# Kernel tuning notes

Measured on AMD Instinct MI355X. Metric: run time of the kernel, lower is better.

## Reference

```python
import jax, jax.numpy as jnp
import numpy as np

C = 512          # in_channels
N1 = 8192        # level-1 nodes
N2 = 131072      # level-2 nodes
N = 1 + N1 + N2  # total nodes (node 0 = root)
E = 1_000_000    # edges
STEP = 10        # ceil(1/ratio), ratio=0.1
K1 = (N1 + STEP - 1) // STEP   # 820 level-1 clusters
K2 = 4 * K1                    # max level-2 clusters (4 centers per parent)
M = 1 + K1 + K2                # coarse node count


def setup_inputs() -> dict:
    key = jax.random.key(0)
    ks = jax.random.split(key, 6)
    x = jax.random.normal(ks[0], (N, C), dtype=jnp.float32)
    edge_index = jax.random.randint(ks[1], (2, E), 0, N, dtype=jnp.int32)
    # fixed hierarchy layout: node 0 root, nodes 1..N1 level-1, rest level-2
    node_type = jnp.concatenate([jnp.zeros(1, jnp.int32),
                                 jnp.ones(N1, jnp.int32),
                                 jnp.full((N2,), 2, jnp.int32)])
    # tree: level-2 nodes point to a level-1 parent (global idx in [1, N1])
    tree = jax.random.randint(ks[2], (N,), 1, N1 + 1, dtype=jnp.int32)
    x_y_index = jax.random.uniform(ks[3], (N, 2), dtype=jnp.float32) * 100.0
    weight_1 = jax.random.normal(ks[4], (1, C), dtype=jnp.float32) * 0.04
    weight_2 = jax.random.normal(ks[5], (1, C), dtype=jnp.float32) * 0.04
    return {"x": x, "edge_index": edge_index, "node_type": node_type,
            "tree": tree, "x_y_index": x_y_index,
            "weight_1": weight_1, "weight_2": weight_2}


def _pair_dist(a, b):
    # a:[m,3], b:[n,3]; xy euclidean distance + |fitness diff| (euclidean_dist)
    dxy = jnp.sqrt(jnp.sum((a[:, None, :2] - b[None, :, :2]) ** 2, axis=-1))
    df = jnp.abs(a[:, None, 2] - b[None, :, 2])
    return dxy + df


def reference(x, edge_index, node_type, tree, x_y_index, weight_1, weight_2):
    x1, x2 = x[1:1 + N1], x[1 + N1:]
    xy1, xy2 = x_y_index[1:1 + N1], x_y_index[1 + N1:]

    # ---- level-1: fitness, threshold selection, cluster by nearest center ----
    f1 = jnp.tanh(jnp.sum(x1 * weight_1, axis=-1) / jnp.linalg.norm(weight_1))
    xyf1 = jnp.concatenate([xy1, f1[:, None]], axis=-1)          # [N1,3]
    order1 = jnp.argsort(f1)
    thr1 = order1[::STEP]                                        # [K1]
    d1 = _pair_dist(xyf1[thr1], xyf1)                            # [K1,N1]
    cluster_1 = jnp.argmin(d1, axis=0).astype(jnp.int32)         # [N1]

    # ---- level-2: fitness, 4 centers per parent cluster, nearest-center ----
    f2 = jnp.tanh(jnp.sum(x2 * weight_2, axis=-1) / jnp.linalg.norm(weight_2))
    xyf2 = jnp.concatenate([xy2, f2[:, None]], axis=-1)          # [N2,3]
    tree2 = tree[1 + N1:]
    parents = cluster_1[tree2 - jnp.min(tree2)]                  # [N2] in [0,K1)
    # pick 4 lowest-fitness members of each parent cluster as centers
    # (static-shape deterministic variant of random.sample over sorted fitness)
    comp_key = parents.astype(jnp.float32) * 4.0 + f2            # fitness in (-1,1)
    order2 = jnp.argsort(comp_key)
    p_sorted = parents[order2]
    counts = jax.ops.segment_sum(jnp.ones((N2,), jnp.int32), parents, K1)
    starts = jnp.concatenate([jnp.zeros(1, jnp.int32), jnp.cumsum(counts)[:-1]])
    rank = jnp.arange(N2, dtype=jnp.int32) - starts[p_sorted]
    row = jnp.where(rank < 4, p_sorted, K1)                      # overflow -> dummy row
    cand = jnp.full((K1 + 1, 4), -1, jnp.int32)
    cand = cand.at[row, jnp.clip(rank, 0, 3)].set(order2.astype(jnp.int32))[:K1]
    valid = cand >= 0                                            # [K1,4]
    cand_xyf = xyf2[jnp.where(valid, cand, 0)]                   # [K1,4,3]
    a = cand_xyf[parents]                                        # [N2,4,3]
    d2 = (jnp.sqrt(jnp.sum((a[..., :2] - xy2[:, None, :]) ** 2, axis=-1))
          + jnp.abs(a[..., 2] - f2[:, None]))
    d2 = jnp.where(valid[parents], d2, jnp.inf)
    local = jnp.argmin(d2, axis=1).astype(jnp.int32)             # [N2] in [0,4)
    cluster_2 = parents * 4 + local                              # [N2]

    # ---- merge cluster ids: [root | level-1 clusters | level-2 clusters] ----
    cluster = jnp.concatenate([jnp.zeros(1, jnp.int32),
                               cluster_1 + 1,
                               cluster_2 + 1 + K1])              # [N] in [0,M)

    # ---- scatter-mean pooling of features and coordinates ----
    cnt = jnp.maximum(jax.ops.segment_sum(jnp.ones((N, 1), x.dtype), cluster, M), 1.0)
    x_pool = jax.ops.segment_sum(x, cluster, M) / cnt            # [M,C]
    new_xy = jax.ops.segment_sum(x_y_index, cluster, M) / cnt    # [M,2]

    # ---- coarsen adjacency (self loops added on fine graph first) ----
    rows = jnp.concatenate([edge_index[0], jnp.arange(N, dtype=jnp.int32)])
    cols = jnp.concatenate([edge_index[1], jnp.arange(N, dtype=jnp.int32)])
    A = jnp.zeros((M, M), x.dtype).at[cluster[rows], cluster[cols]].add(1.0)

    new_node_type = jnp.concatenate([jnp.zeros(1, jnp.int32),
                                     jnp.ones(K1, jnp.int32),
                                     jnp.full((K2,), 2, jnp.int32)])
    new_tree = jnp.concatenate([jnp.full((1,), -1, jnp.int32),
                                jnp.zeros(K1, jnp.int32),
                                jnp.repeat(jnp.arange(1, K1 + 1, dtype=jnp.int32), 4)])
    fitness = jnp.concatenate([jnp.zeros(1, x.dtype), f1, f2])
    batch = jnp.zeros((M,), jnp.int32)
    return x_pool, A, batch, cluster, new_node_type, new_tree, fitness, new_xy
```

## Files before the change

kernel.cpp:

```cpp
#include <hip/hip_runtime.h>
#include <cstdint>
#include <cstddef>
#include <math.h>

#define C_     512
#define N1_    8192
#define N2_    131072
#define NTOT   139265
#define E_     1000000
#define K1_    820
#define K2_    3280
#define M_     4101
#define NB2    256
#define NBM    273

#define OFF_XPOOL   0ull
#define OFF_A       2099712ull
#define OFF_BATCH   18917913ull
#define OFF_CLUSTER 18922014ull
#define OFF_NNT     19061279ull
#define OFF_NTREE   19065380ull
#define OFF_FIT     19069481ull
#define OFF_NXY     19208746ull
#define OUT_TOTAL   19216948ull


__global__ void k_zero4(float4* __restrict__ p, long n4, float* __restrict__ tail, int ntail,
                        float* __restrict__ out) {
    long i = (long)blockIdx.x * blockDim.x + threadIdx.x;
    long stride = (long)gridDim.x * blockDim.x;
    float4 z = make_float4(0.f, 0.f, 0.f, 0.f);
    for (long k = i; k < n4; k += stride) p[k] = z;
    if (blockIdx.x == 0 && threadIdx.x < ntail) tail[threadIdx.x] = 0.f;
    if (i < M_) {
        out[OFF_NNT + i] = (i == 0) ? 0.0f : (i <= K1_ ? 1.0f : 2.0f);
        out[OFF_NTREE + i] = (i == 0) ? -1.0f : (i <= K1_ ? 0.0f : (float)(1 + (i - 1 - K1_) / 4));
        out[OFF_BATCH + i] = 0.0f;
        if (i == 0) out[OFF_FIT] = 0.0f;
    }
}

__device__ __forceinline__ float pairwise_combine(float r) {
    float o;
    o = __shfl_xor(r, 1, 64);  r = __fadd_rn(r, o);
    o = __shfl_xor(r, 2, 64);  r = __fadd_rn(r, o);
    o = __shfl_xor(r, 4, 64);  r = __fadd_rn(r, o);
    o = __shfl_xor(r, 8, 64);  r = __fadd_rn(r, o);
    o = __shfl_xor(r, 16, 64); r = __fadd_rn(r, o);
    return r;
}

__global__ void k_fit(const float* __restrict__ x, const float* __restrict__ w,
                      int rowOff, float* __restrict__ fs, float* __restrict__ fitOut) {
    __shared__ float wbuf[C_];
    __shared__ float xbuf[8][C_];
    for (int j = threadIdx.x; j < C_; j += 256) wbuf[j] = w[j];
    int wv = threadIdx.x >> 6, lane = threadIdx.x & 63;
    int rowA = blockIdx.x * 8 + wv * 2;
    const float4* rA = (const float4*)(x + (size_t)(rowOff + rowA) * C_);
    const float4* rB = (const float4*)(x + (size_t)(rowOff + rowA + 1) * C_);
    float4* xa = (float4*)xbuf[wv * 2];
    float4* xb = (float4*)xbuf[wv * 2 + 1];
    xa[lane] = rA[lane];
    xa[lane + 64] = rA[lane + 64];
    xb[lane] = rB[lane];
    xb[lane + 64] = rB[lane + 64];
    __syncthreads();
    int hl = lane & 31;
    int base = (hl >> 3) * 128 + (hl & 7);
    const float* xr = xbuf[wv * 2 + (lane >> 5)];
    float nv = wbuf[base];
    float nr = __fmul_rn(nv, nv);
    float r = __fmul_rn(xr[base], wbuf[base]);
    #pragma unroll
    for (int i = 1; i < 16; ++i) {
        int c = base + 8 * i;
        float u = wbuf[c];
        nr = __fadd_rn(nr, __fmul_rn(u, u));
        r = __fadd_rn(r, __fmul_rn(xr[c], u));
    }
    nr = pairwise_combine(nr);
    r = pairwise_combine(r);
    if (hl == 0) {
        float nrm = __fsqrt_rn(nr);
        float q = __fdiv_rn(r, nrm);
        float f = (float)tanh((double)q);
        int gw = rowA + (lane >> 5);
        fs[gw] = f;
        fitOut[gw] = f;
    }
}

#define RJ 512
__global__ void k_rank_partial(const float* __restrict__ f1s, int* __restrict__ rank) {
    __shared__ float buf[RJ];
    int i = blockIdx.x * 256 + threadIdx.x;
    int jbase = blockIdx.y * RJ;
    for (int j = threadIdx.x; j < RJ; j += 256) buf[j] = f1s[jbase + j];
    float fi = f1s[i];
    __syncthreads();
    int r = 0;
    #pragma unroll 8
    for (int j = 0; j < RJ; ++j) {
        float fj = buf[j];
        int jj = jbase + j;
        r += (int)((fj < fi) || (fj == fi && jj < i));
    }
    atomicAdd(&rank[i], r);
}

__global__ void k_thr(const int* __restrict__ rank, const float* __restrict__ xy,
                      const float* __restrict__ f1s, float* __restrict__ thrXYF) {
    int i = blockIdx.x * blockDim.x + threadIdx.x;
    if (i >= N1_) return;
    int r = rank[i];
    if (r % 10 == 0) {
        int k = r / 10;
        thrXYF[3 * k + 0] = xy[(size_t)(1 + i) * 2 + 0];
        thrXYF[3 * k + 1] = xy[(size_t)(1 + i) * 2 + 1];
        thrXYF[3 * k + 2] = f1s[i];
    }
}

__device__ __forceinline__ float pair_dist_f32(float ax, float ay, float af,
                                               float bx, float by, float bf) {
    float dx = __fsub_rn(ax, bx);
    float dy = __fsub_rn(ay, by);
    float dx2 = __fmul_rn(dx, dx);
    float dy2 = __fmul_rn(dy, dy);
    float ss = __fadd_rn(dx2, dy2);
    float dxy = __fsqrt_rn(ss);
    float df = fabsf(__fsub_rn(af, bf));
    return __fadd_rn(dxy, df);
}

__global__ void k_cluster1(const float* __restrict__ xy, const float* __restrict__ f1s,
                           const float* __restrict__ thrXYF,
                           int* __restrict__ cluster1, int* __restrict__ clusterAll,
                           float* __restrict__ outCluster, int* __restrict__ cntM) {
    __shared__ float t[K1_ * 3];
    for (int j = threadIdx.x; j < K1_ * 3; j += blockDim.x) t[j] = thrXYF[j];
    __syncthreads();
    if (blockIdx.x == 0 && threadIdx.x == 0) {
        clusterAll[0] = 0; outCluster[0] = 0.0f;
        atomicAdd(&cntM[0], 1);
    }
    int gw = blockIdx.x * (blockDim.x >> 6) + (threadIdx.x >> 6);
    int lane = threadIdx.x & 63;
    if (gw >= N1_) return;
    float xi = xy[(size_t)(1 + gw) * 2 + 0];
    float yi = xy[(size_t)(1 + gw) * 2 + 1];
    float fi = f1s[gw];
    float best = INFINITY; int bk = 0x7fffffff;
    for (int k = lane; k < K1_; k += 64) {
        float d = pair_dist_f32(t[3 * k + 0], t[3 * k + 1], t[3 * k + 2], xi, yi, fi);
        if (d < best || (d == best && k < bk)) { best = d; bk = k; }
    }
    for (int off = 32; off > 0; off >>= 1) {
        float ob = __shfl_down(best, off, 64);
        int ok = __shfl_down(bk, off, 64);
        if (ob < best || (ob == best && ok < bk)) { best = ob; bk = ok; }
    }
    if (lane == 0) {
        cluster1[gw] = bk;
        clusterAll[1 + gw] = bk + 1;
        outCluster[1 + gw] = (float)(bk + 1);
        atomicAdd(&cntM[bk + 1], 1);
    }
}

__global__ void k_mintree(const int* __restrict__ tree, int* __restrict__ minTree) {
    int i = blockIdx.x * blockDim.x + threadIdx.x;
    if (i >= N2_) return;
    int v = tree[1 + N1_ + i];
    for (int off = 32; off > 0; off >>= 1) v = min(v, __shfl_down(v, off, 64));
    if ((threadIdx.x & 63) == 0) atomicMin(minTree, v);
}

__global__ void k_parents(const int* __restrict__ tree, const int* __restrict__ cluster1,
                          const int* __restrict__ minTree,
                          int* __restrict__ parents, int* __restrict__ countP) {
    int i = blockIdx.x * blockDim.x + threadIdx.x;
    if (i >= N2_) return;
    int p = cluster1[tree[1 + N1_ + i] - minTree[0]];
    parents[i] = p;
    atomicAdd(&countP[p], 1);
}

__global__ void k_scan(const int* __restrict__ cnt, int* __restrict__ start, int n) {
    __shared__ int partial[1024];
    int t = threadIdx.x;
    int per = (n + 1023) / 1024;
    int lo = t * per;
    int hi = lo + per; if (hi > n) hi = n;
    int s = 0;
    if (lo < n) for (int i = lo; i < hi; ++i) s += cnt[i];
    partial[t] = s;
    __syncthreads();
    for (int off = 1; off < 1024; off <<= 1) {
        int v = (t >= off) ? partial[t - off] : 0;
        __syncthreads();
        partial[t] += v;
        __syncthreads();
    }
    int base = (t > 0) ? partial[t - 1] : 0;
    if (lo < n) for (int i = lo; i < hi; ++i) { start[i] = base; base += cnt[i]; }
    if (t == 1023) start[n] = partial[1023];
}

__global__ void kA_count(const int* __restrict__ parents, int* __restrict__ bc) {
    __shared__ int hist[K1_];
    for (int j = threadIdx.x; j < K1_; j += 512) hist[j] = 0;
    __syncthreads();
    int i = blockIdx.x * 512 + threadIdx.x;
    atomicAdd(&hist[parents[i]], 1);
    __syncthreads();
    for (int j = threadIdx.x; j < K1_; j += 512) bc[(size_t)j * NB2 + blockIdx.x] = hist[j];
}

__global__ void kA_scan(const int* __restrict__ startP, int* __restrict__ bc) {
    int p = blockIdx.x * 256 + threadIdx.x;
    if (p >= K1_) return;
    int run = startP[p];
    int* row = bc + (size_t)p * NB2;
    for (int b = 0; b < NB2; ++b) { int t = row[b]; row[b] = run; run += t; }
}

__global__ void kA_place(const int* __restrict__ parents, const int* __restrict__ bc,
                         int* __restrict__ plist) {
    __shared__ int par[512];
    int i = blockIdx.x * 512 + threadIdx.x;
    int p = parents[i];
    par[threadIdx.x] = p;
    __syncthreads();
    int rank = 0;
    for (int j = 0; j < (int)threadIdx.x; ++j) rank += (par[j] == p);
    plist[bc[(size_t)p * NB2 + blockIdx.x] + rank] = i;
}

__global__ void kM_count(const int* __restrict__ clusterAll, int* __restrict__ bc) {
    __shared__ int hist[M_];
    for (int j = threadIdx.x; j < M_; j += 512) hist[j] = 0;
    __syncthreads();
    int i = blockIdx.x * 512 + threadIdx.x;
    if (i < NTOT) atomicAdd(&hist[clusterAll[i]], 1);
    __syncthreads();
    for (int j = threadIdx.x; j < M_; j += 512) bc[(size_t)j * NBM + blockIdx.x] = hist[j];
}

__global__ void kM_scan(const int* __restrict__ startM, int* __restrict__ bc) {
    int c = blockIdx.x * 256 + threadIdx.x;
    if (c >= M_) return;
    int run = startM[c];
    int* row = bc + (size_t)c * NBM;
    for (int b = 0; b < NBM; ++b) { int t = row[b]; row[b] = run; run += t; }
}

__global__ void kM_place(const int* __restrict__ clusterAll, const int* __restrict__ bc,
                         int* __restrict__ lst) {
    __shared__ int par[512];
    int i = blockIdx.x * 512 + threadIdx.x;
    int c = (i < NTOT) ? clusterAll[i] : -1;
    par[threadIdx.x] = c;
    __syncthreads();
    if (i >= NTOT) return;
    int rank = 0;
    for (int j = 0; j < (int)threadIdx.x; ++j) rank += (par[j] == c);
    lst[bc[(size_t)c * NBM + blockIdx.x] + rank] = i;
}

__global__ void k_top4(const int* __restrict__ startP, const int* __restrict__ plist,
                       const float* __restrict__ f2s, int* __restrict__ cand) {
    int p = blockIdx.x * (blockDim.x >> 6) + (threadIdx.x >> 6);
    int lane = threadIdx.x & 63;
    if (p >= K1_) return;
    int lo = startP[p], hi = startP[p + 1];
    float base = (float)(4 * p);
    float bk[4] = {INFINITY, INFINITY, INFINITY, INFINITY};
    int bi[4] = {-1, -1, -1, -1};
    for (int q = lo + lane; q < hi; q += 64) {
        int idx = plist[q];
        float key = __fadd_rn(base, f2s[idx]);
        for (int j = 0; j < 4; ++j) {
            bool less = (key < bk[j]) || (key == bk[j] && (unsigned)idx < (unsigned)bi[j]);
            if (less) {
                for (int r = 3; r > j; --r) { bk[r] = bk[r - 1]; bi[r] = bi[r - 1]; }
                bk[j] = key; bi[j] = idx;
                break;
            }
        }
    }
    for (int off = 1; off < 64; off <<= 1) {
        float ok_[4]; int oi[4];
        for (int j = 0; j < 4; ++j) {
            ok_[j] = __shfl_xor(bk[j], off, 64);
            oi[j]  = __shfl_xor(bi[j], off, 64);
        }
        float nk[4]; int ni[4];
        int ia = 0, ib = 0;
        for (int j = 0; j < 4; ++j) {
            bool takeA = (bk[ia] < ok_[ib]) ||
                         (bk[ia] == ok_[ib] && (unsigned)bi[ia] <= (unsigned)oi[ib]);
            if (takeA) { nk[j] = bk[ia]; ni[j] = bi[ia]; ++ia; }
            else       { nk[j] = ok_[ib]; ni[j] = oi[ib]; ++ib; }
        }
        for (int j = 0; j < 4; ++j) { bk[j] = nk[j]; bi[j] = ni[j]; }
    }
    if (lane == 0) {
        for (int j = 0; j < 4; ++j) cand[4 * p + j] = bi[j];
    }
}

__global__ void k_cluster2(const float* __restrict__ xy, const float* __restrict__ f2s,
                           const int* __restrict__ parents, const int* __restrict__ cand,
                           int* __restrict__ clusterAll, float* __restrict__ outCluster,
                           int* __restrict__ cntM) {
    int i = blockIdx.x * blockDim.x + threadIdx.x;
    if (i >= N2_) return;
    int p = parents[i];
    float xi = xy[(size_t)(1 + N1_ + i) * 2 + 0];
    float yi = xy[(size_t)(1 + N1_ + i) * 2 + 1];
    float fi = f2s[i];
    float best = INFINITY; int bj = 0;
    for (int j = 0; j < 4; ++j) {
        int cidx = cand[4 * p + j];
        float d;
        if (cidx < 0) {
            d = INFINITY;
        } else {
            float ax = xy[(size_t)(1 + N1_ + cidx) * 2 + 0];
            float ay = xy[(size_t)(1 + N1_ + cidx) * 2 + 1];
            float af = f2s[cidx];
            d = pair_dist_f32(ax, ay, af, xi, yi, fi);
        }
        if (d < best) { best = d; bj = j; }
    }
    int c2 = p * 4 + bj;
    int c = c2 + 1 + K1_;
    clusterAll[1 + N1_ + i] = c;
    outCluster[1 + N1_ + i] = (float)c;
    atomicAdd(&cntM[c], 1);
}

__global__ void k_pool(const float* __restrict__ x, const float* __restrict__ xy,
                       const int* __restrict__ startM, const int* __restrict__ clusterList,
                       float* __restrict__ out) {
    int m = blockIdx.x;
    int lo = startM[m], hi = startM[m + 1];
    int t = threadIdx.x;
    double s0 = 0.0, s1 = 0.0, s2 = 0.0, s3 = 0.0, sx = 0.0, sy = 0.0;
    int q = lo;
    for (; q + 1 < hi; q += 2) {
        int n0 = clusterList[q];
        int n1 = clusterList[q + 1];
        float4 a = ((const float4*)(x + (size_t)n0 * C_))[t];
        float4 b = ((const float4*)(x + (size_t)n1 * C_))[t];
        s0 += (double)a.x; s1 += (double)a.y; s2 += (double)a.z; s3 += (double)a.w;
        s0 += (double)b.x; s1 += (double)b.y; s2 += (double)b.z; s3 += (double)b.w;
        if (t == 0) sx += (double)xy[(size_t)n0 * 2 + 0] + (double)xy[(size_t)n1 * 2 + 0];
        if (t == 1) sy += (double)xy[(size_t)n0 * 2 + 1] + (double)xy[(size_t)n1 * 2 + 1];
    }
    if (q < hi) {
        int n0 = clusterList[q];
        float4 a = ((const float4*)(x + (size_t)n0 * C_))[t];
        s0 += (double)a.x; s1 += (double)a.y; s2 += (double)a.z; s3 += (double)a.w;
        if (t == 0) sx += (double)xy[(size_t)n0 * 2 + 0];
        if (t == 1) sy += (double)xy[(size_t)n0 * 2 + 1];
    }
    double cnt = (double)((hi - lo) > 0 ? (hi - lo) : 1);
    float4* xp = (float4*)(out + OFF_XPOOL + (size_t)m * C_);
    xp[t] = make_float4((float)(s0 / cnt), (float)(s1 / cnt),
                        (float)(s2 / cnt), (float)(s3 / cnt));
    if (t == 0) out[OFF_NXY + 2 * (size_t)m + 0] = (float)(sx / cnt);
    if (t == 1) out[OFF_NXY + 2 * (size_t)m + 1] = (float)(sy / cnt);
}

__global__ void k_edges(const int* __restrict__ ei, const int* __restrict__ clusterAll,
                        float* __restrict__ A) {
    int i = blockIdx.x * blockDim.x + threadIdx.x;
    if (i < E_) {
        int r = clusterAll[ei[i]];
        int c = clusterAll[ei[E_ + i]];
        atomicAdd(&A[(size_t)r * M_ + c], 1.0f);
    } else {
        int n = i - E_;
        if (n < NTOT) {
            int c = clusterAll[n];
            atomicAdd(&A[(size_t)c * M_ + c], 1.0f);
        }
    }
}

extern "C" void kernel_launch(void* const* d_in, const int* in_sizes, int n_in,
                              void* d_out, int out_size, void* d_ws, size_t ws_size,
                              hipStream_t stream) {
    const float* x    = (const float*)d_in[0];
    const int*   ei   = (const int*)d_in[1];
    const int*   tree = (const int*)d_in[3];
    const float* xy   = (const float*)d_in[4];
    const float* w1   = (const float*)d_in[5];
    const float* w2   = (const float*)d_in[6];
    float* out = (float*)d_out;

    char* p = (char*)d_ws;
    auto alloc = [&](size_t nbytes) -> char* {
        char* r = p;
        p += (nbytes + 255) & ~(size_t)255;
        return r;
    };
    float*  f1s        = (float*)alloc((size_t)N1_ * 4);
    float*  f2s        = (float*)alloc((size_t)N2_ * 4);
    float*  thrXYF     = (float*)alloc((size_t)K1_ * 3 * 4);
    int*    cluster1   = (int*)alloc((size_t)N1_ * 4);
    int*    clusterAll = (int*)alloc((size_t)NTOT * 4);
    int*    parentsA   = (int*)alloc((size_t)N2_ * 4);
    int*    plist      = (int*)alloc((size_t)N2_ * 4);
    int*    clusterLst = (int*)alloc((size_t)NTOT * 4);
    int*    startP     = (int*)alloc((size_t)(K1_ + 1) * 4);
    int*    startM     = (int*)alloc((size_t)(M_ + 1) * 4);
    int*    bcP        = (int*)alloc((size_t)K1_ * NB2 * 4);
    int*    bcM        = (int*)alloc((size_t)M_ * NBM * 4);
    size_t zeroInts = (size_t)(K1_ + M_ + N1_);
    char*   zeroBlk    = alloc(zeroInts * 4);
    int*    countP     = (int*)zeroBlk;
    int*    cntM       = countP + K1_;
    int*    rankArr    = cntM + M_;
    int*    cand       = (int*)alloc((size_t)K1_ * 4 * 4);
    int*    minTree    = (int*)alloc(4);

    hipMemsetAsync(zeroBlk, 0, zeroInts * 4, stream);
    hipMemsetAsync(minTree, 0x7F, 4, stream);

    {
        long nA = (long)M_ * M_;
        long n4 = nA / 4;
        int ntail = (int)(nA - n4 * 4);
        float* A = out + OFF_A;
        k_zero4<<<4096, 256, 0, stream>>>((float4*)A, n4, A + n4 * 4, ntail, out);
    }

    k_fit<<<N1_ / 8, 256, 0, stream>>>(x, w1, 1, f1s, out + OFF_FIT + 1);
    k_fit<<<N2_ / 8, 256, 0, stream>>>(x, w2, 1 + N1_, f2s, out + OFF_FIT + 1 + N1_);
    {
        dim3 g(N1_ / 256, N1_ / RJ);
        k_rank_partial<<<g, 256, 0, stream>>>(f1s, rankArr);
    }
    k_thr<<<N1_ / 256, 256, 0, stream>>>(rankArr, xy, f1s, thrXYF);
    k_cluster1<<<N1_ / 4, 256, 0, stream>>>(xy, f1s, thrXYF, cluster1, clusterAll,
                                            out + OFF_CLUSTER, cntM);
    k_mintree<<<N2_ / 256, 256, 0, stream>>>(tree, minTree);
    k_parents<<<N2_ / 256, 256, 0, stream>>>(tree, cluster1, minTree, parentsA, countP);
    k_scan<<<1, 1024, 0, stream>>>(countP, startP, K1_);
    kA_count<<<NB2, 512, 0, stream>>>(parentsA, bcP);
    kA_scan<<<(K1_ + 255) / 256, 256, 0, stream>>>(startP, bcP);
    kA_place<<<NB2, 512, 0, stream>>>(parentsA, bcP, plist);
    k_top4<<<(K1_ + 3) / 4, 256, 0, stream>>>(startP, plist, f2s, cand);
    k_cluster2<<<N2_ / 256, 256, 0, stream>>>(xy, f2s, parentsA, cand, clusterAll,
                                              out + OFF_CLUSTER, cntM);
    k_scan<<<1, 1024, 0, stream>>>(cntM, startM, M_);
    kM_count<<<NBM, 512, 0, stream>>>(clusterAll, bcM);
    kM_scan<<<(M_ + 255) / 256, 256, 0, stream>>>(startM, bcM);
    kM_place<<<NBM, 512, 0, stream>>>(clusterAll, bcM, clusterLst);
    k_pool<<<M_, 128, 0, stream>>>(x, xy, startM, clusterLst, out);
    k_edges<<<(E_ + NTOT + 255) / 256, 256, 0, stream>>>(ei, clusterAll, out + OFF_A);
}
```

Measured before the change: 798.3 us.

## Fuse whole pipeline into one persistent kernel with software grid barriers

Replaces roughly twenty separate kernel launches with one persistent kernel of 240 blocks. Stages are separated by atomic-counter grid barriers. Along the way it overlaps A-matrix zeroing and the min-tree reduction with the fitness pass, replaces the count-then-scan steps with flattened chunked scans, and runs edge scatter and pooling back to back. This removes launch gaps and tail effects. The cost is reduced parallelism in some stages (240 blocks), barrier spin overhead, and deadlock if not all blocks are co-resident.

```diff
diff --git a/kernel.cpp b/kernel.cpp
--- a/kernel.cpp
+++ b/kernel.cpp
@@ -13,6 +13,19 @@
 #define M_     4101
 #define NB2    256
 #define NBM    273
+#define FLATP  209920
+#define CHP    820
+#define FLATM  1119573
+#define CHM    4374
+#define NCHS   256
+
+#define G_     240
+#define BLK_   512
+#define FITB   210
+#define ZB     30
+#define ZTOT   15360
+#define NG16   8704
+#define PADC   544
 
 #define OFF_XPOOL   0ull
 #define OFF_A       2099712ull
@@ -25,19 +38,36 @@
 #define OUT_TOTAL   19216948ull
 
 
-__global__ void k_zero4(float4* __restrict__ p, long n4, float* __restrict__ tail, int ntail,
-                        float* __restrict__ out) {
-    long i = (long)blockIdx.x * blockDim.x + threadIdx.x;
-    long stride = (long)gridDim.x * blockDim.x;
-    float4 z = make_float4(0.f, 0.f, 0.f, 0.f);
-    for (long k = i; k < n4; k += stride) p[k] = z;
-    if (blockIdx.x == 0 && threadIdx.x < ntail) tail[threadIdx.x] = 0.f;
-    if (i < M_) {
-        out[OFF_NNT + i] = (i == 0) ? 0.0f : (i <= K1_ ? 1.0f : 2.0f);
-        out[OFF_NTREE + i] = (i == 0) ? -1.0f : (i <= K1_ ? 0.0f : (float)(1 + (i - 1 - K1_) / 4));
-        out[OFF_BATCH + i] = 0.0f;
-        if (i == 0) out[OFF_FIT] = 0.0f;
-    }
+struct MegaArgs {
+    const float* x; const int* ei; const int* tree; const float* xy;
+    const float* w1; const float* w2;
+    float* out;
+    float* f1s; float* f2s; float* thrXYF;
+    int* cluster1; int* clusterAll; int* parentsA; int* plist; int* clusterLst;
+    int* bcP; int* bcM;
+    int* totP; int* coffP; int* totM; int* coffM;
+    int* rankArr; int* minTreeNeg;
+    int* cand;
+    int* barCnt; int* barGen;
+};
+
+__device__ __forceinline__ void gbar(int* cnt, int* gen) {
+    __syncthreads();
+    if (threadIdx.x == 0) {
+        __threadfence();
+        int g = __hip_atomic_load(gen, __ATOMIC_RELAXED, __HIP_MEMORY_SCOPE_AGENT);
+        int old = __hip_atomic_fetch_add(cnt, 1, __ATOMIC_ACQ_REL, __HIP_MEMORY_SCOPE_AGENT);
+        if (old == (int)gridDim.x - 1) {
+            __hip_atomic_store(cnt, 0, __ATOMIC_RELAXED, __HIP_MEMORY_SCOPE_AGENT);
+            __hip_atomic_fetch_add(gen, 1, __ATOMIC_RELEASE, __HIP_MEMORY_SCOPE_AGENT);
+        } else {
+            while (__hip_atomic_load(gen, __ATOMIC_RELAXED, __HIP_MEMORY_SCOPE_AGENT) == g) {
+                __builtin_amdgcn_s_sleep(1);
+            }
+        }
+        __threadfence();
+    }
+    __syncthreads();
 }
 
 __device__ __forceinline__ float pairwise_combine(float r) {
@@ -48,78 +78,6 @@
     o = __shfl_xor(r, 8, 64);  r = __fadd_rn(r, o);
     o = __shfl_xor(r, 16, 64); r = __fadd_rn(r, o);
     return r;
-}
-
-__global__ void k_fit(const float* __restrict__ x, const float* __restrict__ w,
-                      int rowOff, float* __restrict__ fs, float* __restrict__ fitOut) {
-    __shared__ float wbuf[C_];
-    __shared__ float xbuf[8][C_];
-    for (int j = threadIdx.x; j < C_; j += 256) wbuf[j] = w[j];
-    int wv = threadIdx.x >> 6, lane = threadIdx.x & 63;
-    int rowA = blockIdx.x * 8 + wv * 2;
-    const float4* rA = (const float4*)(x + (size_t)(rowOff + rowA) * C_);
-    const float4* rB = (const float4*)(x + (size_t)(rowOff + rowA + 1) * C_);
-    float4* xa = (float4*)xbuf[wv * 2];
-    float4* xb = (float4*)xbuf[wv * 2 + 1];
-    xa[lane] = rA[lane];
-    xa[lane + 64] = rA[lane + 64];
-    xb[lane] = rB[lane];
-    xb[lane + 64] = rB[lane + 64];
-    __syncthreads();
-    int hl = lane & 31;
-    int base = (hl >> 3) * 128 + (hl & 7);
-    const float* xr = xbuf[wv * 2 + (lane >> 5)];
-    float nv = wbuf[base];
-    float nr = __fmul_rn(nv, nv);
-    float r = __fmul_rn(xr[base], wbuf[base]);
-    #pragma unroll
-    for (int i = 1; i < 16; ++i) {
-        int c = base + 8 * i;
-        float u = wbuf[c];
-        nr = __fadd_rn(nr, __fmul_rn(u, u));
-        r = __fadd_rn(r, __fmul_rn(xr[c], u));
-    }
-    nr = pairwise_combine(nr);
-    r = pairwise_combine(r);
-    if (hl == 0) {
-        float nrm = __fsqrt_rn(nr);
-        float q = __fdiv_rn(r, nrm);
-        float f = (float)tanh((double)q);
-        int gw = rowA + (lane >> 5);
-        fs[gw] = f;
-        fitOut[gw] = f;
-    }
-}
-
-#define RJ 512
-__global__ void k_rank_partial(const float* __restrict__ f1s, int* __restrict__ rank) {
-    __shared__ float buf[RJ];
-    int i = blockIdx.x * 256 + threadIdx.x;
-    int jbase = blockIdx.y * RJ;
-    for (int j = threadIdx.x; j < RJ; j += 256) buf[j] = f1s[jbase + j];
-    float fi = f1s[i];
-    __syncthreads();
-    int r = 0;
-    #pragma unroll 8
-    for (int j = 0; j < RJ; ++j) {
-        float fj = buf[j];
-        int jj = jbase + j;
-        r += (int)((fj < fi) || (fj == fi && jj < i));
-    }
-    atomicAdd(&rank[i], r);
-}
-
-__global__ void k_thr(const int* __restrict__ rank, const float* __restrict__ xy,
-                      const float* __restrict__ f1s, float* __restrict__ thrXYF) {
-    int i = blockIdx.x * blockDim.x + threadIdx.x;
-    if (i >= N1_) return;
-    int r = rank[i];
-    if (r % 10 == 0) {
-        int k = r / 10;
-        thrXYF[3 * k + 0] = xy[(size_t)(1 + i) * 2 + 0];
-        thrXYF[3 * k + 1] = xy[(size_t)(1 + i) * 2 + 1];
-        thrXYF[3 * k + 2] = f1s[i];
-    }
 }
 
 __device__ __forceinline__ float pair_dist_f32(float ax, float ay, float af,
@@ -134,259 +92,416 @@
     return __fadd_rn(dxy, df);
 }
 
-__global__ void k_cluster1(const float* __restrict__ xy, const float* __restrict__ f1s,
-                           const float* __restrict__ thrXYF,
-                           int* __restrict__ cluster1, int* __restrict__ clusterAll,
-                           float* __restrict__ outCluster, int* __restrict__ cntM) {
-    __shared__ float t[K1_ * 3];
-    for (int j = threadIdx.x; j < K1_ * 3; j += blockDim.x) t[j] = thrXYF[j];
+__device__ __forceinline__ int block_incl_scan512(int v, int* sm) {
+    sm[threadIdx.x] = v;
     __syncthreads();
-    if (blockIdx.x == 0 && threadIdx.x == 0) {
-        clusterAll[0] = 0; outCluster[0] = 0.0f;
-        atomicAdd(&cntM[0], 1);
-    }
-    int gw = blockIdx.x * (blockDim.x >> 6) + (threadIdx.x >> 6);
-    int lane = threadIdx.x & 63;
-    if (gw >= N1_) return;
-    float xi = xy[(size_t)(1 + gw) * 2 + 0];
-    float yi = xy[(size_t)(1 + gw) * 2 + 1];
-    float fi = f1s[gw];
-    float best = INFINITY; int bk = 0x7fffffff;
-    for (int k = lane; k < K1_; k += 64) {
-        float d = pair_dist_f32(t[3 * k + 0], t[3 * k + 1], t[3 * k + 2], xi, yi, fi);
-        if (d < best || (d == best && k < bk)) { best = d; bk = k; }
-    }
-    for (int off = 32; off > 0; off >>= 1) {
-        float ob = __shfl_down(best, off, 64);
-        int ok = __shfl_down(bk, off, 64);
-        if (ob < best || (ob == best && ok < bk)) { best = ob; bk = ok; }
-    }
-    if (lane == 0) {
-        cluster1[gw] = bk;
-        clusterAll[1 + gw] = bk + 1;
-        outCluster[1 + gw] = (float)(bk + 1);
-        atomicAdd(&cntM[bk + 1], 1);
-    }
+    for (int off = 1; off < 512; off <<= 1) {
+        int y = ((int)threadIdx.x >= off) ? sm[threadIdx.x - off] : 0;
+        __syncthreads();
+        sm[threadIdx.x] += y;
+        __syncthreads();
+    }
+    return sm[threadIdx.x];
 }
 
-__global__ void k_mintree(const int* __restrict__ tree, int* __restrict__ minTree) {
-    int i = blockIdx.x * blockDim.x + threadIdx.x;
-    if (i >= N2_) return;
-    int v = tree[1 + N1_ + i];
-    for (int off = 32; off > 0; off >>= 1) v = min(v, __shfl_down(v, off, 64));
-    if ((threadIdx.x & 63) == 0) atomicMin(minTree, v);
-}
-
-__global__ void k_parents(const int* __restrict__ tree, const int* __restrict__ cluster1,
-                          const int* __restrict__ minTree,
-                          int* __restrict__ parents, int* __restrict__ countP) {
-    int i = blockIdx.x * blockDim.x + threadIdx.x;
-    if (i >= N2_) return;
-    int p = cluster1[tree[1 + N1_ + i] - minTree[0]];
-    parents[i] = p;
-    atomicAdd(&countP[p], 1);
-}
-
-__global__ void k_scan(const int* __restrict__ cnt, int* __restrict__ start, int n) {
-    __shared__ int partial[1024];
-    int t = threadIdx.x;
-    int per = (n + 1023) / 1024;
-    int lo = t * per;
-    int hi = lo + per; if (hi > n) hi = n;
-    int s = 0;
-    if (lo < n) for (int i = lo; i < hi; ++i) s += cnt[i];
-    partial[t] = s;
-    __syncthreads();
-    for (int off = 1; off < 1024; off <<= 1) {
-        int v = (t >= off) ? partial[t - off] : 0;
-        __syncthreads();
-        partial[t] += v;
-        __syncthreads();
-    }
-    int base = (t > 0) ? partial[t - 1] : 0;
-    if (lo < n) for (int i = lo; i < hi; ++i) { start[i] = base; base += cnt[i]; }
-    if (t == 1023) start[n] = partial[1023];
-}
-
-__global__ void kA_count(const int* __restrict__ parents, int* __restrict__ bc) {
-    __shared__ int hist[K1_];
-    for (int j = threadIdx.x; j < K1_; j += 512) hist[j] = 0;
-    __syncthreads();
-    int i = blockIdx.x * 512 + threadIdx.x;
-    atomicAdd(&hist[parents[i]], 1);
-    __syncthreads();
-    for (int j = threadIdx.x; j < K1_; j += 512) bc[(size_t)j * NB2 + blockIdx.x] = hist[j];
-}
-
-__global__ void kA_scan(const int* __restrict__ startP, int* __restrict__ bc) {
-    int p = blockIdx.x * 256 + threadIdx.x;
-    if (p >= K1_) return;
-    int run = startP[p];
-    int* row = bc + (size_t)p * NB2;
-    for (int b = 0; b < NB2; ++b) { int t = row[b]; row[b] = run; run += t; }
-}
-
-__global__ void kA_place(const int* __restrict__ parents, const int* __restrict__ bc,
-                         int* __restrict__ plist) {
-    __shared__ int par[512];
-    int i = blockIdx.x * 512 + threadIdx.x;
-    int p = parents[i];
-    par[threadIdx.x] = p;
-    __syncthreads();
-    int rank = 0;
-    for (int j = 0; j < (int)threadIdx.x; ++j) rank += (par[j] == p);
-    plist[bc[(size_t)p * NB2 + blockIdx.x] + rank] = i;
-}
-
-__global__ void kM_count(const int* __restrict__ clusterAll, int* __restrict__ bc) {
-    __shared__ int hist[M_];
-    for (int j = threadIdx.x; j < M_; j += 512) hist[j] = 0;
-    __syncthreads();
-    int i = blockIdx.x * 512 + threadIdx.x;
-    if (i < NTOT) atomicAdd(&hist[clusterAll[i]], 1);
-    __syncthreads();
-    for (int j = threadIdx.x; j < M_; j += 512) bc[(size_t)j * NBM + blockIdx.x] = hist[j];
-}
-
-__global__ void kM_scan(const int* __restrict__ startM, int* __restrict__ bc) {
-    int c = blockIdx.x * 256 + threadIdx.x;
-    if (c >= M_) return;
-    int run = startM[c];
-    int* row = bc + (size_t)c * NBM;
-    for (int b = 0; b < NBM; ++b) { int t = row[b]; row[b] = run; run += t; }
-}
-
-__global__ void kM_place(const int* __restrict__ clusterAll, const int* __restrict__ bc,
-                         int* __restrict__ lst) {
-    __shared__ int par[512];
-    int i = blockIdx.x * 512 + threadIdx.x;
-    int c = (i < NTOT) ? clusterAll[i] : -1;
-    par[threadIdx.x] = c;
-    __syncthreads();
-    if (i >= NTOT) return;
-    int rank = 0;
-    for (int j = 0; j < (int)threadIdx.x; ++j) rank += (par[j] == c);
-    lst[bc[(size_t)c * NBM + blockIdx.x] + rank] = i;
-}
-
-__global__ void k_top4(const int* __restrict__ startP, const int* __restrict__ plist,
-                       const float* __restrict__ f2s, int* __restrict__ cand) {
-    int p = blockIdx.x * (blockDim.x >> 6) + (threadIdx.x >> 6);
-    int lane = threadIdx.x & 63;
-    if (p >= K1_) return;
-    int lo = startP[p], hi = startP[p + 1];
-    float base = (float)(4 * p);
-    float bk[4] = {INFINITY, INFINITY, INFINITY, INFINITY};
-    int bi[4] = {-1, -1, -1, -1};
-    for (int q = lo + lane; q < hi; q += 64) {
-        int idx = plist[q];
-        float key = __fadd_rn(base, f2s[idx]);
+__global__ void __launch_bounds__(BLK_, 2) k_mega(MegaArgs a) {
+    __shared__ float smem_f[PADC * 17];
+    int* smem_i = (int*)smem_f;
+    const int tid = threadIdx.x;
+    const int bid = blockIdx.x;
+    const int wv = tid >> 6, lane = tid & 63;
+
+    if ((bid & 7) != 3) {
+        int fidx = bid - (bid >> 3) - (((bid & 7) > 3) ? 1 : 0);
+        float* wbuf = smem_f;
+        float* xbuf = smem_f + PADC;
+        for (int g = fidx; g < NG16; g += FITB) {
+            const float* w = (g < 512) ? a.w1 : a.w2;
+            if (tid < 128) {
+                float4 v = ((const float4*)w)[tid];
+                ((float4*)wbuf)[((tid >> 5) * 34) + (tid & 31)] = v;
+            }
+            {
+                int r0 = 2 * wv, r1 = r0 + 1;
+                const float4* rA = (const float4*)(a.x + (size_t)(1 + 16 * g + r0) * C_);
+                const float4* rB = (const float4*)(a.x + (size_t)(1 + 16 * g + r1) * C_);
+                float4* xa = (float4*)(xbuf + (size_t)r0 * PADC);
+                float4* xb = (float4*)(xbuf + (size_t)r1 * PADC);
+                int j0 = lane, j1 = lane + 64;
+                int d0 = ((j0 >> 5) * 34) + (j0 & 31);
+                int d1 = ((j1 >> 5) * 34) + (j1 & 31);
+                xa[d0] = rA[j0]; xa[d1] = rA[j1];
+                xb[d0] = rB[j0]; xb[d1] = rB[j1];
+            }
+            __syncthreads();
+            {
+                int hl = lane & 31;
+                int basep = ((hl >> 3) * 136) + (hl & 7);
+                const float* xr = xbuf + (size_t)(2 * wv + (lane >> 5)) * PADC;
+                float nv = wbuf[basep];
+                float nr = __fmul_rn(nv, nv);
+                float r = __fmul_rn(xr[basep], wbuf[basep]);
+                #pragma unroll
+                for (int i = 1; i < 16; ++i) {
+                    int c = basep + 8 * i;
+                    float u = wbuf[c];
+                    nr = __fadd_rn(nr, __fmul_rn(u, u));
+                    r = __fadd_rn(r, __fmul_rn(xr[c], u));
+                }
+                nr = pairwise_combine(nr);
+                r = pairwise_combine(r);
+                if (hl == 0) {
+                    float nrm = __fsqrt_rn(nr);
+                    float q = __fdiv_rn(r, nrm);
+                    float f = (float)tanh((double)q);
+                    int row16 = 16 * g + 2 * wv + (lane >> 5);
+                    if (row16 < N1_) a.f1s[row16] = f;
+                    else             a.f2s[row16 - N1_] = f;
+                    a.out[OFF_FIT + 1 + row16] = f;
+                }
+            }
+            __syncthreads();
+        }
+    } else {
+        int ztid = (bid >> 3) * BLK_ + tid;
+        float* A = a.out + OFF_A;
+        const long n4 = ((long)M_ * M_) >> 2;
+        float4 z = make_float4(0.f, 0.f, 0.f, 0.f);
+        for (long k4 = ztid; k4 < n4; k4 += ZTOT) ((float4*)A)[k4] = z;
+        if (ztid == 0) {
+            A[(size_t)n4 * 4] = 0.f;
+            a.clusterAll[0] = 0;
+            a.out[OFF_CLUSTER] = 0.0f;
+            a.out[OFF_FIT] = 0.0f;
+        }
+        if (ztid < M_) {
+            a.out[OFF_NNT + ztid] = (ztid == 0) ? 0.0f : (ztid <= K1_ ? 1.0f : 2.0f);
+            a.out[OFF_NTREE + ztid] = (ztid == 0) ? -1.0f
+                                    : (ztid <= K1_ ? 0.0f : (float)(1 + (ztid - 1 - K1_) / 4));
+            a.out[OFF_BATCH + ztid] = 0.0f;
+        }
+        int u = 0;
+        for (int i = ztid; i < N2_; i += ZTOT) {
+            int v = a.tree[1 + N1_ + i];
+            u = max(u, 0x7FFFFFFF - v);
+        }
+        for (int off = 32; off > 0; off >>= 1) u = max(u, __shfl_down(u, off, 64));
+        if (lane == 0) atomicMax(a.minTreeNeg, u);
+    }
+    gbar(a.barCnt, a.barGen);
+
+    for (int vb = bid; vb < 256; vb += G_) {
+        float* buf = smem_f;
+        int i = (vb >> 4) * 512 + tid;
+        int jbase = (vb & 15) * 512;
+        buf[tid] = a.f1s[jbase + tid];
+        float fi = a.f1s[i];
+        __syncthreads();
+        int r = 0;
+        #pragma unroll 8
+        for (int j = 0; j < 512; ++j) {
+            float fj = buf[j];
+            int jj = jbase + j;
+            r += (int)((fj < fi) || (fj == fi && jj < i));
+        }
+        atomicAdd(&a.rankArr[i], r);
+        __syncthreads();
+    }
+    gbar(a.barCnt, a.barGen);
+
+    for (int i = bid * BLK_ + tid; i < N1_; i += G_ * BLK_) {
+        int r = a.rankArr[i];
+        if (r % 10 == 0) {
+            int k = r / 10;
+            a.thrXYF[3 * k + 0] = a.xy[(size_t)(1 + i) * 2 + 0];
+            a.thrXYF[3 * k + 1] = a.xy[(size_t)(1 + i) * 2 + 1];
+            a.thrXYF[3 * k + 2] = a.f1s[i];
+        }
+    }
+    gbar(a.barCnt, a.barGen);
+
+    {
+        float* t = smem_f;
+        for (int j = tid; j < K1_ * 3; j += BLK_) t[j] = a.thrXYF[j];
+        __syncthreads();
+        for (int gw = bid * 8 + wv; gw < N1_; gw += G_ * 8) {
+            float xi = a.xy[(size_t)(1 + gw) * 2 + 0];
+            float yi = a.xy[(size_t)(1 + gw) * 2 + 1];
+            float fi = a.f1s[gw];
+            float best = INFINITY; int bk = 0x7fffffff;
+            for (int k = lane; k < K1_; k += 64) {
+                float d = pair_dist_f32(t[3 * k + 0], t[3 * k + 1], t[3 * k + 2], xi, yi, fi);
+                if (d < best || (d == best && k < bk)) { best = d; bk = k; }
+            }
+            for (int off = 32; off > 0; off >>= 1) {
+                float ob = __shfl_down(best, off, 64);
+                int ok = __shfl_down(bk, off, 64);
+                if (ob < best || (ob == best && ok < bk)) { best = ob; bk = ok; }
+            }
+            if (lane == 0) {
+                a.cluster1[gw] = bk;
+                a.clusterAll[1 + gw] = bk + 1;
+                a.out[OFF_CLUSTER + 1 + gw] = (float)(bk + 1);
+            }
+        }
+    }
+    gbar(a.barCnt, a.barGen);
+
+    {
+        int mt = 0x7FFFFFFF - a.minTreeNeg[0];
+        for (int i = bid * BLK_ + tid; i < N2_; i += G_ * BLK_) {
+            a.parentsA[i] = a.cluster1[a.tree[1 + N1_ + i] - mt];
+        }
+    }
+    gbar(a.barCnt, a.barGen);
+
+    for (int ch = bid; ch < NB2; ch += G_) {
+        int* hist = smem_i;
+        for (int j = tid; j < K1_; j += BLK_) hist[j] = 0;
+        __syncthreads();
+        int i = ch * 512 + tid;
+        atomicAdd(&hist[a.parentsA[i]], 1);
+        __syncthreads();
+        for (int j = tid; j < K1_; j += BLK_) a.bcP[(size_t)j * NB2 + ch] = hist[j];
+        __syncthreads();
+    }
+    gbar(a.barCnt, a.barGen);
+
+    for (int ch = bid; ch < NCHS; ch += G_) {
+        int base = ch * CHP;
+        int e0 = 2 * tid, e1 = 2 * tid + 1;
+        int v0 = (e0 < CHP) ? a.bcP[base + e0] : 0;
+        int v1 = (e1 < CHP) ? a.bcP[base + e1] : 0;
+        int s = v0 + v1;
+        int incl = block_incl_scan512(s, smem_i);
+        int excl = incl - s;
+        if (e0 < CHP) a.bcP[base + e0] = excl;
+        if (e1 < CHP) a.bcP[base + e1] = excl + v0;
+        if (tid == 511) a.totP[ch] = incl;
+        __syncthreads();
+    }
+    gbar(a.barCnt, a.barGen);
+
+    if (bid == 0) {
+        int v = (tid < NCHS) ? a.totP[tid] : 0;
+        int incl = block_incl_scan512(v, smem_i);
+        if (tid < NCHS) a.coffP[tid] = incl - v;
+    }
+    gbar(a.barCnt, a.barGen);
+
+    for (int ch = bid; ch < NB2; ch += G_) {
+        int* par = smem_i;
+        int i = ch * 512 + tid;
+        int p = a.parentsA[i];
+        par[tid] = p;
+        __syncthreads();
+        int rnk = 0;
+        for (int j = 0; j < tid; ++j) rnk += (par[j] == p);
+        int flat = p * NB2 + ch;
+        a.plist[a.bcP[flat] + a.coffP[flat / CHP] + rnk] = i;
+        __syncthreads();
+    }
+    gbar(a.barCnt, a.barGen);
+
+    for (int p = bid * 8 + wv; p < K1_; p += G_ * 8) {
+        int f0 = p * NB2;
+        int f1 = (p + 1) * NB2;
+        int lo = a.bcP[f0] + a.coffP[f0 / CHP];
+        int hi = (p + 1 < K1_) ? (a.bcP[f1] + a.coffP[f1 / CHP]) : N2_;
+        float basek = (float)(4 * p);
+        float bk[4] = {INFINITY, INFINITY, INFINITY, INFINITY};
+        int bi[4] = {-1, -1, -1, -1};
+        for (int q = lo + lane; q < hi; q += 64) {
+            int idx = a.plist[q];
+            float key = __fadd_rn(basek, a.f2s[idx]);
+            for (int j = 0; j < 4; ++j) {
+                bool less = (key < bk[j]) || (key == bk[j] && (unsigned)idx < (unsigned)bi[j]);
+                if (less) {
+                    for (int r = 3; r > j; --r) { bk[r] = bk[r - 1]; bi[r] = bi[r - 1]; }
+                    bk[j] = key; bi[j] = idx;
+                    break;
+                }
+            }
+        }
+        for (int off = 1; off < 64; off <<= 1) {
+            float ok_[4]; int oi[4];
+            for (int j = 0; j < 4; ++j) {
+                ok_[j] = __shfl_xor(bk[j], off, 64);
+                oi[j]  = __shfl_xor(bi[j], off, 64);
+            }
+            float nk[4]; int ni[4];
+            int ia = 0, ib2 = 0;
+            for (int j = 0; j < 4; ++j) {
+                bool takeA = (bk[ia] < ok_[ib2]) ||
+                             (bk[ia] == ok_[ib2] && (unsigned)bi[ia] <= (unsigned)oi[ib2]);
+                if (takeA) { nk[j] = bk[ia]; ni[j] = bi[ia]; ++ia; }
+                else       { nk[j] = ok_[ib2]; ni[j] = oi[ib2]; ++ib2; }
+            }
+            for (int j = 0; j < 4; ++j) { bk[j] = nk[j]; bi[j] = ni[j]; }
+        }
+        if (lane == 0) {
+            for (int j = 0; j < 4; ++j) a.cand[4 * p + j] = bi[j];
+        }
+    }
+    gbar(a.barCnt, a.barGen);
+
+    for (int i = bid * BLK_ + tid; i < N2_; i += G_ * BLK_) {
+        int p = a.parentsA[i];
+        float xi = a.xy[(size_t)(1 + N1_ + i) * 2 + 0];
+        float yi = a.xy[(size_t)(1 + N1_ + i) * 2 + 1];
+        float fi = a.f2s[i];
+        float best = INFINITY; int bj = 0;
         for (int j = 0; j < 4; ++j) {
-            bool less = (key < bk[j]) || (key == bk[j] && (unsigned)idx < (unsigned)bi[j]);
-            if (less) {
-                for (int r = 3; r > j; --r) { bk[r] = bk[r - 1]; bi[r] = bi[r - 1]; }
-                bk[j] = key; bi[j] = idx;
-                break;
-            }
-        }
-    }
-    for (int off = 1; off < 64; off <<= 1) {
-        float ok_[4]; int oi[4];
-        for (int j = 0; j < 4; ++j) {
-            ok_[j] = __shfl_xor(bk[j], off, 64);
-            oi[j]  = __shfl_xor(bi[j], off, 64);
-        }
-        float nk[4]; int ni[4];
-        int ia = 0, ib = 0;
-        for (int j = 0; j < 4; ++j) {
-            bool takeA = (bk[ia] < ok_[ib]) ||
-                         (bk[ia] == ok_[ib] && (unsigned)bi[ia] <= (unsigned)oi[ib]);
-            if (takeA) { nk[j] = bk[ia]; ni[j] = bi[ia]; ++ia; }
-            else       { nk[j] = ok_[ib]; ni[j] = oi[ib]; ++ib; }
-        }
-        for (int j = 0; j < 4; ++j) { bk[j] = nk[j]; bi[j] = ni[j]; }
-    }
-    if (lane == 0) {
-        for (int j = 0; j < 4; ++j) cand[4 * p + j] = bi[j];
-    }
-}
-
-__global__ void k_cluster2(const float* __restrict__ xy, const float* __restrict__ f2s,
-                           const int* __restrict__ parents, const int* __restrict__ cand,
-                           int* __restrict__ clusterAll, float* __restrict__ outCluster,
-                           int* __restrict__ cntM) {
-    int i = blockIdx.x * blockDim.x + threadIdx.x;
-    if (i >= N2_) return;
-    int p = parents[i];
-    float xi = xy[(size_t)(1 + N1_ + i) * 2 + 0];
-    float yi = xy[(size_t)(1 + N1_ + i) * 2 + 1];
-    float fi = f2s[i];
-    float best = INFINITY; int bj = 0;
-    for (int j = 0; j < 4; ++j) {
-        int cidx = cand[4 * p + j];
-        float d;
-        if (cidx < 0) {
-            d = INFINITY;
-        } else {
-            float ax = xy[(size_t)(1 + N1_ + cidx) * 2 + 0];
-            float ay = xy[(size_t)(1 + N1_ + cidx) * 2 + 1];
-            float af = f2s[cidx];
-            d = pair_dist_f32(ax, ay, af, xi, yi, fi);
-        }
-        if (d < best) { best = d; bj = j; }
-    }
-    int c2 = p * 4 + bj;
-    int c = c2 + 1 + K1_;
-    clusterAll[1 + N1_ + i] = c;
-    outCluster[1 + N1_ + i] = (float)c;
-    atomicAdd(&cntM[c], 1);
-}
-
-__global__ void k_pool(const float* __restrict__ x, const float* __restrict__ xy,
-                       const int* __restrict__ startM, const int* __restrict__ clusterList,
-                       float* __restrict__ out) {
-    int m = blockIdx.x;
-    int lo = startM[m], hi = startM[m + 1];
-    int t = threadIdx.x;
-    double s0 = 0.0, s1 = 0.0, s2 = 0.0, s3 = 0.0, sx = 0.0, sy = 0.0;
-    int q = lo;
-    for (; q + 1 < hi; q += 2) {
-        int n0 = clusterList[q];
-        int n1 = clusterList[q + 1];
-        float4 a = ((const float4*)(x + (size_t)n0 * C_))[t];
-        float4 b = ((const float4*)(x + (size_t)n1 * C_))[t];
-        s0 += (double)a.x; s1 += (double)a.y; s2 += (double)a.z; s3 += (double)a.w;
-        s0 += (double)b.x; s1 += (double)b.y; s2 += (double)b.z; s3 += (double)b.w;
-        if (t == 0) sx += (double)xy[(size_t)n0 * 2 + 0] + (double)xy[(size_t)n1 * 2 + 0];
-        if (t == 1) sy += (double)xy[(size_t)n0 * 2 + 1] + (double)xy[(size_t)n1 * 2 + 1];
-    }
-    if (q < hi) {
-        int n0 = clusterList[q];
-        float4 a = ((const float4*)(x + (size_t)n0 * C_))[t];
-        s0 += (double)a.x; s1 += (double)a.y; s2 += (double)a.z; s3 += (double)a.w;
-        if (t == 0) sx += (double)xy[(size_t)n0 * 2 + 0];
-        if (t == 1) sy += (double)xy[(size_t)n0 * 2 + 1];
-    }
-    double cnt = (double)((hi - lo) > 0 ? (hi - lo) : 1);
-    float4* xp = (float4*)(out + OFF_XPOOL + (size_t)m * C_);
-    xp[t] = make_float4((float)(s0 / cnt), (float)(s1 / cnt),
-                        (float)(s2 / cnt), (float)(s3 / cnt));
-    if (t == 0) out[OFF_NXY + 2 * (size_t)m + 0] = (float)(sx / cnt);
-    if (t == 1) out[OFF_NXY + 2 * (size_t)m + 1] = (float)(sy / cnt);
-}
-
-__global__ void k_edges(const int* __restrict__ ei, const int* __restrict__ clusterAll,
-                        float* __restrict__ A) {
-    int i = blockIdx.x * blockDim.x + threadIdx.x;
-    if (i < E_) {
-        int r = clusterAll[ei[i]];
-        int c = clusterAll[ei[E_ + i]];
-        atomicAdd(&A[(size_t)r * M_ + c], 1.0f);
-    } else {
-        int n = i - E_;
-        if (n < NTOT) {
-            int c = clusterAll[n];
-            atomicAdd(&A[(size_t)c * M_ + c], 1.0f);
+            int cidx = a.cand[4 * p + j];
+            float d;
+            if (cidx < 0) {
+                d = INFINITY;
+            } else {
+                float ax = a.xy[(size_t)(1 + N1_ + cidx) * 2 + 0];
+                float ay = a.xy[(size_t)(1 + N1_ + cidx) * 2 + 1];
+                float af = a.f2s[cidx];
+                d = pair_dist_f32(ax, ay, af, xi, yi, fi);
+            }
+            if (d < best) { best = d; bj = j; }
+        }
+        int c = p * 4 + bj + 1 + K1_;
+        a.clusterAll[1 + N1_ + i] = c;
+        a.out[OFF_CLUSTER + 1 + N1_ + i] = (float)c;
+    }
+    gbar(a.barCnt, a.barGen);
+
+    for (int ch = bid; ch < NBM; ch += G_) {
+        int* hist = smem_i;
+        for (int j = tid; j < M_; j += BLK_) hist[j] = 0;
+        __syncthreads();
+        int i = ch * 512 + tid;
+        if (i < NTOT) atomicAdd(&hist[a.clusterAll[i]], 1);
+        __syncthreads();
+        for (int j = tid; j < M_; j += BLK_) a.bcM[(size_t)j * NBM + ch] = hist[j];
+        __syncthreads();
+    }
+    gbar(a.barCnt, a.barGen);
+
+    for (int ch = bid; ch < NCHS; ch += G_) {
+        int base = ch * CHM;
+        int ce = min(base + CHM, FLATM);
+        int g0 = base + tid * 9;
+        int v[9]; int s = 0;
+        #pragma unroll
+        for (int k = 0; k < 9; ++k) {
+            int idx = g0 + k;
+            v[k] = (idx < ce) ? a.bcM[idx] : 0;
+            s += v[k];
+        }
+        int incl = block_incl_scan512(s, smem_i);
+        int excl = incl - s;
+        int run = excl;
+        #pragma unroll
+        for (int k = 0; k < 9; ++k) {
+            int idx = g0 + k;
+            if (idx < ce) { a.bcM[idx] = run; run += v[k]; }
+        }
+        if (tid == 511) a.totM[ch] = incl;
+        __syncthreads();
+    }
+    gbar(a.barCnt, a.barGen);
+
+    if (bid == 0) {
+        int v = (tid < NCHS) ? a.totM[tid] : 0;
+        int incl = block_incl_scan512(v, smem_i);
+        if (tid < NCHS) a.coffM[tid] = incl - v;
+    }
+    gbar(a.barCnt, a.barGen);
+
+    for (int ch = bid; ch < NBM; ch += G_) {
+        int* par = smem_i;
+        int i = ch * 512 + tid;
+        int c = (i < NTOT) ? a.clusterAll[i] : -1;
+        par[tid] = c;
+        __syncthreads();
+        if (i < NTOT) {
+            int rnk = 0;
+            for (int j = 0; j < tid; ++j) rnk += (par[j] == c);
+            int flat = c * NBM + ch;
+            a.clusterLst[a.bcM[flat] + a.coffM[flat / CHM] + rnk] = i;
+        }
+        __syncthreads();
+    }
+    gbar(a.barCnt, a.barGen);
+
+    {
+        float* A = a.out + OFF_A;
+        int gtid = bid * BLK_ + tid;
+        for (long i = gtid; i < (long)E_ + NTOT; i += (long)G_ * BLK_) {
+            if (i < E_) {
+                int r = a.clusterAll[a.ei[i]];
+                int c = a.clusterAll[a.ei[E_ + i]];
+                atomicAdd(&A[(size_t)r * M_ + c], 1.0f);
+            } else {
+                int n = (int)(i - E_);
+                int c = a.clusterAll[n];
+                atomicAdd(&A[(size_t)c * M_ + c], 1.0f);
+            }
+        }
+    }
+    {
+        int unit = bid * 4 + (tid >> 7);
+        int tsub = tid & 127;
+        for (int m = unit; m < M_; m += G_ * 4) {
+            int fl0 = m * NBM;
+            int lo = a.bcM[fl0] + a.coffM[fl0 / CHM];
+            int hi;
+            if (m + 1 < M_) {
+                int fl1 = (m + 1) * NBM;
+                hi = a.bcM[fl1] + a.coffM[fl1 / CHM];
+            } else hi = NTOT;
+            double s0 = 0.0, s1 = 0.0, s2 = 0.0, s3 = 0.0, sx = 0.0, sy = 0.0;
+            int q = lo;
+            for (; q + 3 < hi; q += 4) {
+                int n0 = a.clusterLst[q];
+                int n1 = a.clusterLst[q + 1];
+                int n2 = a.clusterLst[q + 2];
+                int n3 = a.clusterLst[q + 3];
+                float4 va = ((const float4*)(a.x + (size_t)n0 * C_))[tsub];
+                float4 vb = ((const float4*)(a.x + (size_t)n1 * C_))[tsub];
+                float4 vc = ((const float4*)(a.x + (size_t)n2 * C_))[tsub];
+                float4 vd = ((const float4*)(a.x + (size_t)n3 * C_))[tsub];
+                s0 += (double)va.x; s1 += (double)va.y; s2 += (double)va.z; s3 += (double)va.w;
+                s0 += (double)vb.x; s1 += (double)vb.y; s2 += (double)vb.z; s3 += (double)vb.w;
+                s0 += (double)vc.x; s1 += (double)vc.y; s2 += (double)vc.z; s3 += (double)vc.w;
+                s0 += (double)vd.x; s1 += (double)vd.y; s2 += (double)vd.z; s3 += (double)vd.w;
+                if (tsub == 0) {
+                    sx += (double)a.xy[(size_t)n0 * 2 + 0] + (double)a.xy[(size_t)n1 * 2 + 0];
+                    sx += (double)a.xy[(size_t)n2 * 2 + 0] + (double)a.xy[(size_t)n3 * 2 + 0];
+                }
+                if (tsub == 1) {
+                    sy += (double)a.xy[(size_t)n0 * 2 + 1] + (double)a.xy[(size_t)n1 * 2 + 1];
+                    sy += (double)a.xy[(size_t)n2 * 2 + 1] + (double)a.xy[(size_t)n3 * 2 + 1];
+                }
+            }
+            for (; q + 1 < hi; q += 2) {
+                int n0 = a.clusterLst[q];
+                int n1 = a.clusterLst[q + 1];
+                float4 va = ((const float4*)(a.x + (size_t)n0 * C_))[tsub];
+                float4 vb = ((const float4*)(a.x + (size_t)n1 * C_))[tsub];
+                s0 += (double)va.x; s1 += (double)va.y; s2 += (double)va.z; s3 += (double)va.w;
+                s0 += (double)vb.x; s1 += (double)vb.y; s2 += (double)vb.z; s3 += (double)vb.w;
+                if (tsub == 0) sx += (double)a.xy[(size_t)n0 * 2 + 0] + (double)a.xy[(size_t)n1 * 2 + 0];
+                if (tsub == 1) sy += (double)a.xy[(size_t)n0 * 2 + 1] + (double)a.xy[(size_t)n1 * 2 + 1];
+            }
+            if (q < hi) {
+                int n0 = a.clusterLst[q];
+                float4 va = ((const float4*)(a.x + (size_t)n0 * C_))[tsub];
+                s0 += (double)va.x; s1 += (double)va.y; s2 += (double)va.z; s3 += (double)va.w;
+                if (tsub == 0) sx += (double)a.xy[(size_t)n0 * 2 + 0];
+                if (tsub == 1) sy += (double)a.xy[(size_t)n0 * 2 + 1];
+            }
+            double cnt = (double)((hi - lo) > 0 ? (hi - lo) : 1);
+            float4* xp = (float4*)(a.out + OFF_XPOOL + (size_t)m * C_);
+            xp[tsub] = make_float4((float)(s0 / cnt), (float)(s1 / cnt),
+                                   (float)(s2 / cnt), (float)(s3 / cnt));
+            if (tsub == 0) a.out[OFF_NXY + 2 * (size_t)m + 0] = (float)(sx / cnt);
+            if (tsub == 1) a.out[OFF_NXY + 2 * (size_t)m + 1] = (float)(sy / cnt);
         }
     }
 }
@@ -416,51 +531,33 @@
     int*    parentsA   = (int*)alloc((size_t)N2_ * 4);
     int*    plist      = (int*)alloc((size_t)N2_ * 4);
     int*    clusterLst = (int*)alloc((size_t)NTOT * 4);
-    int*    startP     = (int*)alloc((size_t)(K1_ + 1) * 4);
-    int*    startM     = (int*)alloc((size_t)(M_ + 1) * 4);
-    int*    bcP        = (int*)alloc((size_t)K1_ * NB2 * 4);
-    int*    bcM        = (int*)alloc((size_t)M_ * NBM * 4);
-    size_t zeroInts = (size_t)(K1_ + M_ + N1_);
+    int*    bcP        = (int*)alloc((size_t)FLATP * 4);
+    int*    bcM        = (int*)alloc((size_t)FLATM * 4);
+    int*    totP       = (int*)alloc(256 * 4);
+    int*    coffP      = (int*)alloc(256 * 4);
+    int*    totM       = (int*)alloc(256 * 4);
+    int*    coffM      = (int*)alloc(256 * 4);
+    size_t zeroInts = (size_t)N1_ + 3;
     char*   zeroBlk    = alloc(zeroInts * 4);
-    int*    countP     = (int*)zeroBlk;
-    int*    cntM       = countP + K1_;
-    int*    rankArr    = cntM + M_;
+    int*    rankArr    = (int*)zeroBlk;
+    int*    minTreeNeg = rankArr + N1_;
+    int*    barCnt     = minTreeNeg + 1;
+    int*    barGen     = barCnt + 1;
     int*    cand       = (int*)alloc((size_t)K1_ * 4 * 4);
-    int*    minTree    = (int*)alloc(4);
 
     hipMemsetAsync(zeroBlk, 0, zeroInts * 4, stream);
-    hipMemsetAsync(minTree, 0x7F, 4, stream);
-
-    {
-        long nA = (long)M_ * M_;
-        long n4 = nA / 4;
-        int ntail = (int)(nA - n4 * 4);
-        float* A = out + OFF_A;
-        k_zero4<<<4096, 256, 0, stream>>>((float4*)A, n4, A + n4 * 4, ntail, out);
-    }
-
-    k_fit<<<N1_ / 8, 256, 0, stream>>>(x, w1, 1, f1s, out + OFF_FIT + 1);
-    k_fit<<<N2_ / 8, 256, 0, stream>>>(x, w2, 1 + N1_, f2s, out + OFF_FIT + 1 + N1_);
-    {
-        dim3 g(N1_ / 256, N1_ / RJ);
-        k_rank_partial<<<g, 256, 0, stream>>>(f1s, rankArr);
-    }
-    k_thr<<<N1_ / 256, 256, 0, stream>>>(rankArr, xy, f1s, thrXYF);
-    k_cluster1<<<N1_ / 4, 256, 0, stream>>>(xy, f1s, thrXYF, cluster1, clusterAll,
-                                            out + OFF_CLUSTER, cntM);
-    k_mintree<<<N2_ / 256, 256, 0, stream>>>(tree, minTree);
-    k_parents<<<N2_ / 256, 256, 0, stream>>>(tree, cluster1, minTree, parentsA, countP);
-    k_scan<<<1, 1024, 0, stream>>>(countP, startP, K1_);
-    kA_count<<<NB2, 512, 0, stream>>>(parentsA, bcP);
-    kA_scan<<<(K1_ + 255) / 256, 256, 0, stream>>>(startP, bcP);
-    kA_place<<<NB2, 512, 0, stream>>>(parentsA, bcP, plist);
-    k_top4<<<(K1_ + 3) / 4, 256, 0, stream>>>(startP, plist, f2s, cand);
-    k_cluster2<<<N2_ / 256, 256, 0, stream>>>(xy, f2s, parentsA, cand, clusterAll,
-                                              out + OFF_CLUSTER, cntM);
-    k_scan<<<1, 1024, 0, stream>>>(cntM, startM, M_);
-    kM_count<<<NBM, 512, 0, stream>>>(clusterAll, bcM);
-    kM_scan<<<(M_ + 255) / 256, 256, 0, stream>>>(startM, bcM);
-    kM_place<<<NBM, 512, 0, stream>>>(clusterAll, bcM, clusterLst);
-    k_pool<<<M_, 128, 0, stream>>>(x, xy, startM, clusterLst, out);
-    k_edges<<<(E_ + NTOT + 255) / 256, 256, 0, stream>>>(ei, clusterAll, out + OFF_A);
+
+    MegaArgs ha;
+    ha.x = x; ha.ei = ei; ha.tree = tree; ha.xy = xy; ha.w1 = w1; ha.w2 = w2;
+    ha.out = out;
+    ha.f1s = f1s; ha.f2s = f2s; ha.thrXYF = thrXYF;
+    ha.cluster1 = cluster1; ha.clusterAll = clusterAll; ha.parentsA = parentsA;
+    ha.plist = plist; ha.clusterLst = clusterLst;
+    ha.bcP = bcP; ha.bcM = bcM;
+    ha.totP = totP; ha.coffP = coffP; ha.totM = totM; ha.coffM = coffM;
+    ha.rankArr = rankArr; ha.minTreeNeg = minTreeNeg;
+    ha.cand = cand;
+    ha.barCnt = barCnt; ha.barGen = barGen;
+
+    k_mega<<<G_, BLK_, 0, stream>>>(ha);
 }
```

New measurement: 1.142 ms. +43.0%, slower.
